# Optimization experiments

Hardware: AMD Instinct MI355X
Metric: run time of the kernel (lower is better)

## Reference

```python
import jax, jax.numpy as jnp
import numpy as np

B, T, H = 4, 2048, 512
HEADS = 8
D = H // HEADS  # head dim = 64


def setup_inputs() -> dict:
    key = jax.random.key(0)
    ks = jax.random.split(key, 5)
    s = 1.0 / np.sqrt(H)
    return {
        "x": jax.random.normal(ks[0], (B, T, H), dtype=jnp.float32),
        "w_qkv": jax.random.uniform(ks[1], (H, 3 * H), dtype=jnp.float32, minval=-s, maxval=s),
        "b_qkv": jax.random.uniform(ks[2], (3 * H,), dtype=jnp.float32, minval=-s, maxval=s),
        "w_proj": jax.random.uniform(ks[3], (H, H), dtype=jnp.float32, minval=-s, maxval=s),
        "b_proj": jax.random.uniform(ks[4], (H,), dtype=jnp.float32, minval=-s, maxval=s),
    }


def reference(x, w_qkv, b_qkv, w_proj, b_proj):
    b, t, h = x.shape
    scale = (h // HEADS) ** (-0.5)
    qkv = (x @ w_qkv + b_qkv).reshape(b, t, 3, HEADS, h // HEADS)
    q, k, v = qkv[:, :, 0], qkv[:, :, 1], qkv[:, :, 2]  # [b,t,heads,d]
    q = q * scale
    scores = jnp.einsum('bthd,bThd->bhtT', q, k)  # [b,heads,t,t]
    weights = jax.nn.softmax(scores, axis=-1)
    attn = jnp.einsum('bhtT,bThd->bthd', weights, v).reshape(b, t, h)
    return attn @ w_proj + b_proj
```

## Files before the change

kernel.cpp:

```cpp
#include <hip/hip_runtime.h>
#include <stdint.h>

typedef unsigned short u16;
typedef __attribute__((ext_vector_type(8))) __bf16 bf16x8;
typedef __attribute__((ext_vector_type(4))) __bf16 bf16x4;
typedef __attribute__((ext_vector_type(4))) float f32x4;
typedef __attribute__((ext_vector_type(2))) unsigned int u32x2;
typedef __attribute__((ext_vector_type(4))) unsigned int u32x4;

#define QSCALE 0.18033688011112042f

__device__ __forceinline__ u16 f2bf(float f) {
    uint32_t u = __builtin_bit_cast(uint32_t, f);
    u = (u + 0x7fffu + ((u >> 16) & 1u)) >> 16;
    return (u16)u;
}
__device__ __forceinline__ float bf2f(u16 h) {
    uint32_t u = ((uint32_t)h) << 16;
    return __builtin_bit_cast(float, u);
}

__device__ __forceinline__ void gl_lds16(const u16* g, u16* l) {
    __builtin_amdgcn_global_load_lds(
        (__attribute__((address_space(1))) uint32_t*)(g),
        (__attribute__((address_space(3))) uint32_t*)(l), 16, 0, 0);
}

__global__ __launch_bounds__(256) void convert_x_k(const float* __restrict__ xf,
                                                   u16* __restrict__ xbf) {
    const size_t v = (size_t)blockIdx.x * 256 + threadIdx.x;
    const f32x4 val = ((const f32x4*)xf)[v];
    u32x2 p;
    p.x = (uint32_t)f2bf(val.x) | ((uint32_t)f2bf(val.y) << 16);
    p.y = (uint32_t)f2bf(val.z) | ((uint32_t)f2bf(val.w) << 16);
    *(u32x2*)&xbf[v * 4] = p;
}

__global__ void transpose_cvt_k(const float* __restrict__ in,
                                u16* __restrict__ out, int R, int C) {
    __shared__ u16 t[64][65];
    const int bx = blockIdx.x << 6, by = blockIdx.y << 6;
    const int tx = threadIdx.x, ty = threadIdx.y;
#pragma unroll
    for (int i = ty; i < 64; i += 8)
        t[i][tx] = f2bf(in[(size_t)(by + i) * C + bx + tx]);
    __syncthreads();
#pragma unroll
    for (int i = ty; i < 64; i += 8) out[(size_t)(bx + i) * R + by + tx] = t[tx][i];
}

template <int EPI>
__global__ __launch_bounds__(256) void gemm_bt_k(
    const u16* __restrict__ A, const u16* __restrict__ Bt,
    const float* __restrict__ bias,
    u16* __restrict__ Qb, u16* __restrict__ Kb, u16* __restrict__ Vt,
    float* __restrict__ OutF) {
    __shared__ u16 lA[2][128 * 32];
    __shared__ u16 lB[2][128 * 32];
    const int tid = threadIdx.x;
    const int w = tid >> 6, l = tid & 63, quad = l >> 4, r = l & 15;
    const int tm = blockIdx.x << 7, tn = blockIdx.y << 7;
    const int wm = (w >> 1) << 6, wn = (w & 1) << 6;
    const int srow = l >> 2, sch = (l & 3) << 3;

    f32x4 acc[4][4];
#pragma unroll
    for (int i = 0; i < 4; ++i)
#pragma unroll
        for (int j = 0; j < 4; ++j) acc[i][j] = (f32x4){0.f, 0.f, 0.f, 0.f};

    auto stage = [&](int b, int kk) {
#pragma unroll
        for (int ii = 0; ii < 2; ++ii) {
            const int rowl = w * 32 + ii * 16;
            gl_lds16(A + (size_t)(tm + rowl + srow) * 512 + kk + sch, &lA[b][rowl * 32]);
            gl_lds16(Bt + (size_t)(tn + rowl + srow) * 512 + kk + sch, &lB[b][rowl * 32]);
        }
    };

    stage(0, 0);
    __syncthreads();

    int cur = 0;
    for (int kk = 0; kk < 512; kk += 32) {
        if (kk + 32 < 512) stage(cur ^ 1, kk + 32);
        bf16x8 af[4], bfr[4];
#pragma unroll
        for (int mi = 0; mi < 4; ++mi)
            af[mi] = *(const bf16x8*)&lA[cur][(wm + mi * 16 + r) * 32 + quad * 8];
#pragma unroll
        for (int ni = 0; ni < 4; ++ni)
            bfr[ni] = *(const bf16x8*)&lB[cur][(wn + ni * 16 + r) * 32 + quad * 8];
#pragma unroll
        for (int mi = 0; mi < 4; ++mi)
#pragma unroll
            for (int ni = 0; ni < 4; ++ni)
                acc[mi][ni] = __builtin_amdgcn_mfma_f32_16x16x32_bf16(
                    af[mi], bfr[ni], acc[mi][ni], 0, 0, 0);
        __syncthreads();
        cur ^= 1;
    }

#pragma unroll
    for (int ni = 0; ni < 4; ++ni) {
        const int n = tn + wn + ni * 16 + r;
        const float bv = bias[n];
        const int which = n >> 9, head = (n >> 6) & 7, d = n & 63;
#pragma unroll
        for (int mi = 0; mi < 4; ++mi) {
#pragma unroll
            for (int i = 0; i < 4; ++i) {
                const int m = tm + wm + mi * 16 + quad * 4 + i;
                const float v = acc[mi][ni][i] + bv;
                if (EPI == 0) {
                    const int bb = m >> 11, t = m & 2047;
                    const int bh = bb * 8 + head;
                    if (which == 0)
                        Qb[((size_t)(bh * 2048 + t) << 6) + d] = f2bf(v * QSCALE);
                    else if (which == 1)
                        Kb[((size_t)(bh * 2048 + t) << 6) + d] = f2bf(v);
                    else
                        Vt[((size_t)(bh * 64 + d) << 11) + t] = f2bf(v);
                } else {
                    OutF[(size_t)m * 512 + n] = v;
                }
            }
        }
    }
}

__global__ __launch_bounds__(256) void attn_k(
    const u16* __restrict__ Qb, const u16* __restrict__ Kb,
    const u16* __restrict__ Vt, u16* __restrict__ attnb) {
    __shared__ u16 lk[2][64 * 64];
    __shared__ u16 lv[2][64 * 64];
    __shared__ u16 lp[4][16 * 64];
    const int tid = threadIdx.x;
    const int w = tid >> 6, l = tid & 63, quad = l >> 4, r = l & 15;
    const int qt = blockIdx.x, bh = blockIdx.y;
    const size_t qbase = (size_t)bh * 2048 + qt * 64;
    const int srl = l >> 3;
    const int sg = (l & 7) ^ srl;

    const bf16x8 qf0 = *(const bf16x8*)&Qb[((qbase + w * 16 + r) << 6) + quad * 8];
    const bf16x8 qf1 = *(const bf16x8*)&Qb[((qbase + w * 16 + r) << 6) + 32 + quad * 8];

    const int rl = r & 7;
    const int rhi = r >> 3;
    const int psw = rl << 3;

    const u32x4 onesu = {0x3F803F80u, 0x3F803F80u, 0x3F803F80u, 0x3F803F80u};
    const bf16x8 vones = __builtin_bit_cast(bf16x8, onesu);

    f32x4 o[4];
#pragma unroll
    for (int i = 0; i < 4; ++i) o[i] = (f32x4){0.f, 0.f, 0.f, 0.f};
    f32x4 osum = (f32x4){0.f, 0.f, 0.f, 0.f};

    auto stage = [&](int b, int kv0) {
#pragma unroll
        for (int ii = 0; ii < 2; ++ii) {
            const int chunk = w * 2 + ii;
            gl_lds16(Kb + ((size_t)(bh * 2048 + kv0 + chunk * 8 + srl) << 6) + sg * 8,
                     &lk[b][chunk * 512]);
            gl_lds16(Vt + (((size_t)(bh * 64 + chunk * 8 + srl)) << 11) + kv0 + sg * 8,
                     &lv[b][chunk * 512]);
        }
    };

    stage(0, 0);
    __syncthreads();

    int cur = 0;
    for (int kv0 = 0; kv0 < 2048; kv0 += 64) {
        if (kv0 + 64 < 2048) stage(cur ^ 1, kv0 + 64);

#pragma unroll
        for (int kt = 0; kt < 4; ++kt) {
            const int base = (kt * 2 + rhi) * 512 + rl * 64;
            const bf16x8 a0 = *(const bf16x8*)&lk[cur][base + (quad ^ rl) * 8];
            const bf16x8 a1 = *(const bf16x8*)&lk[cur][base + ((quad ^ rl) ^ 4) * 8];
            f32x4 z = (f32x4){0.f, 0.f, 0.f, 0.f};
            __builtin_amdgcn_s_setprio(1);
            z = __builtin_amdgcn_mfma_f32_16x16x32_bf16(a0, qf0, z, 0, 0, 0);
            z = __builtin_amdgcn_mfma_f32_16x16x32_bf16(a1, qf1, z, 0, 0, 0);
            __builtin_amdgcn_s_setprio(0);
            const uint32_t u0 =
                __builtin_bit_cast(uint32_t, __builtin_amdgcn_exp2f(z[0])) + 0x8000u;
            const uint32_t u1 =
                __builtin_bit_cast(uint32_t, __builtin_amdgcn_exp2f(z[1])) + 0x8000u;
            const uint32_t u2 =
                __builtin_bit_cast(uint32_t, __builtin_amdgcn_exp2f(z[2])) + 0x8000u;
            const uint32_t u3 =
                __builtin_bit_cast(uint32_t, __builtin_amdgcn_exp2f(z[3])) + 0x8000u;
            const uint32_t lo = __builtin_amdgcn_perm(u1, u0, 0x07060302u);
            const uint32_t hi = __builtin_amdgcn_perm(u3, u2, 0x07060302u);
            const uint64_t both = (uint64_t)lo | ((uint64_t)hi << 32);
            *(bf16x4*)&lp[w][r * 64 + ((kt * 16 + quad * 4) ^ psw)] =
                __builtin_bit_cast(bf16x4, both);
        }

        asm volatile("s_waitcnt lgkmcnt(0)" ::: "memory");

        __builtin_amdgcn_s_setprio(1);
#pragma unroll
        for (int h = 0; h < 2; ++h) {
            const bf16x8 ap =
                *(const bf16x8*)&lp[w][r * 64 + ((h * 32 + quad * 8) ^ psw)];
#pragma unroll
            for (int dt = 0; dt < 4; ++dt) {
                const int baseV = (dt * 2 + rhi) * 512 + rl * 64;
                const bf16x8 bv =
                    *(const bf16x8*)&lv[cur][baseV + ((h * 4 + quad) ^ rl) * 8];
                o[dt] = __builtin_amdgcn_mfma_f32_16x16x32_bf16(ap, bv, o[dt], 0, 0, 0);
            }
            osum = __builtin_amdgcn_mfma_f32_16x16x32_bf16(ap, vones, osum, 0, 0, 0);
        }
        __builtin_amdgcn_s_setprio(0);

        __syncthreads();
        cur ^= 1;
    }

    const int bb = bh >> 3, head = bh & 7;
#pragma unroll
    for (int i = 0; i < 4; ++i) {
        const float inv = __builtin_amdgcn_rcpf(osum[i]);
        const int row = bb * 2048 + qt * 64 + w * 16 + quad * 4 + i;
#pragma unroll
        for (int dt = 0; dt < 4; ++dt)
            attnb[(size_t)row * 512 + head * 64 + dt * 16 + r] = f2bf(o[dt][i] * inv);
    }
}

extern "C" void kernel_launch(void* const* d_in, const int* in_sizes, int n_in,
                              void* d_out, int out_size, void* d_ws, size_t ws_size,
                              hipStream_t stream) {
    const float *x = nullptr, *wq = nullptr, *bq = nullptr, *wp = nullptr, *bp = nullptr;
    for (int i = 0; i < n_in; ++i) {
        switch (in_sizes[i]) {
            case 4194304: x  = (const float*)d_in[i]; break;
            case 786432:  wq = (const float*)d_in[i]; break;
            case 1536:    bq = (const float*)d_in[i]; break;
            case 262144:  wp = (const float*)d_in[i]; break;
            case 512:     bp = (const float*)d_in[i]; break;
        }
    }
    if (!x || !wq || !bq || !wp || !bp) {
        x = (const float*)d_in[0]; wq = (const float*)d_in[1];
        bq = (const float*)d_in[2]; wp = (const float*)d_in[3];
        bp = (const float*)d_in[4];
    }
    float* out = (float*)d_out;

    char* ws = (char*)d_ws;
    u16* attnb  = (u16*)(ws + 0);
    u16* wqkvT  = (u16*)(ws + 0);
    u16* Qb     = (u16*)(ws + 8388608);
    u16* wprojT = (u16*)(ws + 8388608);
    u16* Kb     = (u16*)(ws + 16777216);
    u16* Vt     = (u16*)(ws + 25165824);
    u16* xbf    = (u16*)d_out;

    convert_x_k<<<dim3(4096), 256, 0, stream>>>(x, xbf);
    transpose_cvt_k<<<dim3(24, 8), dim3(64, 8), 0, stream>>>(wq, wqkvT, 512, 1536);
    gemm_bt_k<0><<<dim3(64, 12), 256, 0, stream>>>(xbf, wqkvT, bq, Qb, Kb, Vt, nullptr);
    attn_k<<<dim3(32, 32), 256, 0, stream>>>(Qb, Kb, Vt, attnb);
    transpose_cvt_k<<<dim3(8, 8), dim3(64, 8), 0, stream>>>(wp, wprojT, 512, 512);
    gemm_bt_k<1><<<dim3(64, 4), 256, 0, stream>>>(attnb, wprojT, bp, nullptr, nullptr,
                                                  nullptr, out);
}
```

Measured before the change: 175.8 us.

## Give each attention wave two 16-row query tiles, halve waves per block

The attention kernel now runs 2 waves per block instead of 4, and each wave handles 32 query rows as two 16-row MFMA tiles. The K and V fragments read from LDS are reused across both query tiles, which halves LDS reads per MFMA, and each wave now stages twice as many K/V chunks. The cost is roughly double the accumulator and Q-fragment registers per wave and fewer waves per block to hide latency, so occupancy and overlap may suffer.

```diff
diff --git a/kernel.cpp b/kernel.cpp
--- a/kernel.cpp
+++ b/kernel.cpp
@@ -129,12 +129,12 @@
     }
 }
 
-__global__ __launch_bounds__(256) void attn_k(
+__global__ __launch_bounds__(128) void attn_k(
     const u16* __restrict__ Qb, const u16* __restrict__ Kb,
     const u16* __restrict__ Vt, u16* __restrict__ attnb) {
     __shared__ u16 lk[2][64 * 64];
     __shared__ u16 lv[2][64 * 64];
-    __shared__ u16 lp[4][16 * 64];
+    __shared__ u16 lp[2][32 * 64];
     const int tid = threadIdx.x;
     const int w = tid >> 6, l = tid & 63, quad = l >> 4, r = l & 15;
     const int qt = blockIdx.x, bh = blockIdx.y;
@@ -142,29 +142,38 @@
     const int srl = l >> 3;
     const int sg = (l & 7) ^ srl;
 
-    const bf16x8 qf0 = *(const bf16x8*)&Qb[((qbase + w * 16 + r) << 6) + quad * 8];
-    const bf16x8 qf1 = *(const bf16x8*)&Qb[((qbase + w * 16 + r) << 6) + 32 + quad * 8];
-
     const int rl = r & 7;
     const int rhi = r >> 3;
     const int psw = rl << 3;
 
+    bf16x8 qf[2][2];
+#pragma unroll
+    for (int qs = 0; qs < 2; ++qs)
+#pragma unroll
+        for (int hf = 0; hf < 2; ++hf)
+            qf[qs][hf] = *(const bf16x8*)&Qb[((qbase + w * 32 + qs * 16 + r) << 6) +
+                                            hf * 32 + quad * 8];
+
     const u32x4 onesu = {0x3F803F80u, 0x3F803F80u, 0x3F803F80u, 0x3F803F80u};
     const bf16x8 vones = __builtin_bit_cast(bf16x8, onesu);
 
-    f32x4 o[4];
-#pragma unroll
-    for (int i = 0; i < 4; ++i) o[i] = (f32x4){0.f, 0.f, 0.f, 0.f};
-    f32x4 osum = (f32x4){0.f, 0.f, 0.f, 0.f};
+    f32x4 o0[4], o1[4];
+#pragma unroll
+    for (int i = 0; i < 4; ++i) {
+        o0[i] = (f32x4){0.f, 0.f, 0.f, 0.f};
+        o1[i] = (f32x4){0.f, 0.f, 0.f, 0.f};
+    }
+    f32x4 osum0 = (f32x4){0.f, 0.f, 0.f, 0.f};
+    f32x4 osum1 = (f32x4){0.f, 0.f, 0.f, 0.f};
 
     auto stage = [&](int b, int kv0) {
 #pragma unroll
-        for (int ii = 0; ii < 2; ++ii) {
-            const int chunk = w * 2 + ii;
-            gl_lds16(Kb + ((size_t)(bh * 2048 + kv0 + chunk * 8 + srl) << 6) + sg * 8,
-                     &lk[b][chunk * 512]);
-            gl_lds16(Vt + (((size_t)(bh * 64 + chunk * 8 + srl)) << 11) + kv0 + sg * 8,
-                     &lv[b][chunk * 512]);
+        for (int ii = 0; ii < 4; ++ii) {
+            const int ck = w * 4 + ii;
+            gl_lds16(Kb + ((size_t)(bh * 2048 + kv0 + ck * 8 + srl) << 6) + sg * 8,
+                     &lk[b][ck * 512]);
+            gl_lds16(Vt + (((size_t)(bh * 64 + ck * 8 + srl)) << 11) + kv0 + sg * 8,
+                     &lv[b][ck * 512]);
         }
     };
 
@@ -180,24 +189,27 @@
             const int base = (kt * 2 + rhi) * 512 + rl * 64;
             const bf16x8 a0 = *(const bf16x8*)&lk[cur][base + (quad ^ rl) * 8];
             const bf16x8 a1 = *(const bf16x8*)&lk[cur][base + ((quad ^ rl) ^ 4) * 8];
-            f32x4 z = (f32x4){0.f, 0.f, 0.f, 0.f};
-            __builtin_amdgcn_s_setprio(1);
-            z = __builtin_amdgcn_mfma_f32_16x16x32_bf16(a0, qf0, z, 0, 0, 0);
-            z = __builtin_amdgcn_mfma_f32_16x16x32_bf16(a1, qf1, z, 0, 0, 0);
-            __builtin_amdgcn_s_setprio(0);
-            const uint32_t u0 =
-                __builtin_bit_cast(uint32_t, __builtin_amdgcn_exp2f(z[0])) + 0x8000u;
-            const uint32_t u1 =
-                __builtin_bit_cast(uint32_t, __builtin_amdgcn_exp2f(z[1])) + 0x8000u;
-            const uint32_t u2 =
-                __builtin_bit_cast(uint32_t, __builtin_amdgcn_exp2f(z[2])) + 0x8000u;
-            const uint32_t u3 =
-                __builtin_bit_cast(uint32_t, __builtin_amdgcn_exp2f(z[3])) + 0x8000u;
-            const uint32_t lo = __builtin_amdgcn_perm(u1, u0, 0x07060302u);
-            const uint32_t hi = __builtin_amdgcn_perm(u3, u2, 0x07060302u);
-            const uint64_t both = (uint64_t)lo | ((uint64_t)hi << 32);
-            *(bf16x4*)&lp[w][r * 64 + ((kt * 16 + quad * 4) ^ psw)] =
-                __builtin_bit_cast(bf16x4, both);
+#pragma unroll
+            for (int qs = 0; qs < 2; ++qs) {
+                f32x4 z = (f32x4){0.f, 0.f, 0.f, 0.f};
+                __builtin_amdgcn_s_setprio(1);
+                z = __builtin_amdgcn_mfma_f32_16x16x32_bf16(a0, qf[qs][0], z, 0, 0, 0);
+                z = __builtin_amdgcn_mfma_f32_16x16x32_bf16(a1, qf[qs][1], z, 0, 0, 0);
+                __builtin_amdgcn_s_setprio(0);
+                const uint32_t u0 =
+                    __builtin_bit_cast(uint32_t, __builtin_amdgcn_exp2f(z[0])) + 0x8000u;
+                const uint32_t u1 =
+                    __builtin_bit_cast(uint32_t, __builtin_amdgcn_exp2f(z[1])) + 0x8000u;
+                const uint32_t u2 =
+                    __builtin_bit_cast(uint32_t, __builtin_amdgcn_exp2f(z[2])) + 0x8000u;
+                const uint32_t u3 =
+                    __builtin_bit_cast(uint32_t, __builtin_amdgcn_exp2f(z[3])) + 0x8000u;
+                const uint32_t lo = __builtin_amdgcn_perm(u1, u0, 0x07060302u);
+                const uint32_t hi = __builtin_amdgcn_perm(u3, u2, 0x07060302u);
+                const uint64_t both = (uint64_t)lo | ((uint64_t)hi << 32);
+                *(bf16x4*)&lp[w][(qs * 16 + r) * 64 + ((kt * 16 + quad * 4) ^ psw)] =
+                    __builtin_bit_cast(bf16x4, both);
+            }
         }
 
         asm volatile("s_waitcnt lgkmcnt(0)" ::: "memory");
@@ -205,16 +217,20 @@
         __builtin_amdgcn_s_setprio(1);
 #pragma unroll
         for (int h = 0; h < 2; ++h) {
-            const bf16x8 ap =
-                *(const bf16x8*)&lp[w][r * 64 + ((h * 32 + quad * 8) ^ psw)];
+            const bf16x8 ap0 =
+                *(const bf16x8*)&lp[w][(r)*64 + ((h * 32 + quad * 8) ^ psw)];
+            const bf16x8 ap1 =
+                *(const bf16x8*)&lp[w][(16 + r) * 64 + ((h * 32 + quad * 8) ^ psw)];
 #pragma unroll
             for (int dt = 0; dt < 4; ++dt) {
                 const int baseV = (dt * 2 + rhi) * 512 + rl * 64;
                 const bf16x8 bv =
                     *(const bf16x8*)&lv[cur][baseV + ((h * 4 + quad) ^ rl) * 8];
-                o[dt] = __builtin_amdgcn_mfma_f32_16x16x32_bf16(ap, bv, o[dt], 0, 0, 0);
+                o0[dt] = __builtin_amdgcn_mfma_f32_16x16x32_bf16(ap0, bv, o0[dt], 0, 0, 0);
+                o1[dt] = __builtin_amdgcn_mfma_f32_16x16x32_bf16(ap1, bv, o1[dt], 0, 0, 0);
             }
-            osum = __builtin_amdgcn_mfma_f32_16x16x32_bf16(ap, vones, osum, 0, 0, 0);
+            osum0 = __builtin_amdgcn_mfma_f32_16x16x32_bf16(ap0, vones, osum0, 0, 0, 0);
+            osum1 = __builtin_amdgcn_mfma_f32_16x16x32_bf16(ap1, vones, osum1, 0, 0, 0);
         }
         __builtin_amdgcn_s_setprio(0);
 
@@ -225,11 +241,15 @@
     const int bb = bh >> 3, head = bh & 7;
 #pragma unroll
     for (int i = 0; i < 4; ++i) {
-        const float inv = __builtin_amdgcn_rcpf(osum[i]);
-        const int row = bb * 2048 + qt * 64 + w * 16 + quad * 4 + i;
-#pragma unroll
-        for (int dt = 0; dt < 4; ++dt)
-            attnb[(size_t)row * 512 + head * 64 + dt * 16 + r] = f2bf(o[dt][i] * inv);
+        const float inv0 = __builtin_amdgcn_rcpf(osum0[i]);
+        const float inv1 = __builtin_amdgcn_rcpf(osum1[i]);
+        const int row0 = bb * 2048 + qt * 64 + w * 32 + quad * 4 + i;
+        const int row1 = row0 + 16;
+#pragma unroll
+        for (int dt = 0; dt < 4; ++dt) {
+            attnb[(size_t)row0 * 512 + head * 64 + dt * 16 + r] = f2bf(o0[dt][i] * inv0);
+            attnb[(size_t)row1 * 512 + head * 64 + dt * 16 + r] = f2bf(o1[dt][i] * inv1);
+        }
     }
 }
 
@@ -265,7 +285,7 @@
     convert_x_k<<<dim3(4096), 256, 0, stream>>>(x, xbf);
     transpose_cvt_k<<<dim3(24, 8), dim3(64, 8), 0, stream>>>(wq, wqkvT, 512, 1536);
     gemm_bt_k<0><<<dim3(64, 12), 256, 0, stream>>>(xbf, wqkvT, bq, Qb, Kb, Vt, nullptr);
-    attn_k<<<dim3(32, 32), 256, 0, stream>>>(Qb, Kb, Vt, attnb);
+    attn_k<<<dim3(32, 32), 128, 0, stream>>>(Qb, Kb, Vt, attnb);
     transpose_cvt_k<<<dim3(8, 8), dim3(64, 8), 0, stream>>>(wp, wprojT, 512, 512);
     gemm_bt_k<1><<<dim3(64, 4), 256, 0, stream>>>(attnb, wprojT, bp, nullptr, nullptr,
                                                   nullptr, out);
```

Result: slower. 179.6 us (+2.1%).
